# Kernel tuning notes

Hardware: AMD Instinct MI355X
Metric: run time of the kernel (lower is better)

## Reference

```python
import jax, jax.numpy as jnp
import numpy as np

SQRT_N = 64  # sqrt_n; padded sequence length n = SQRT_N**2 = 4096


def _perm(x, r):
    # rearrange '... (m n) -> ... (n m)' with m = n = r
    return x.reshape(*x.shape[:-1], r, r).swapaxes(-1, -2).reshape(x.shape)


def _blockdiag_matmul(x, w):
    # torch.einsum('bnm,...bm->...bn', w, x.view(..., b, m)).reshape(x.shape)
    b, _, m = w.shape
    xv = x.reshape(*x.shape[:-1], b, m)
    return jnp.einsum('bnm,...bm->...bn', w, xv).reshape(x.shape)


def _monarch(x, L, R, r):
    x = _perm(x, r)
    x = _blockdiag_matmul(x, L)
    x = _perm(x, r)
    x = _blockdiag_matmul(x, R)
    return _perm(x, r)


def setup_inputs() -> dict:
    key = jax.random.key(0)
    ks = jax.random.split(key, 9)
    B, S, H, D = 8, 4096, 8, 64
    r = SQRT_N
    bound_b = 1.0 / r
    # kaiming_uniform_(a=sqrt(5)) on a (r, r, r) tensor: fan_in = r*r,
    # gain = sqrt(2/(1+5)) = sqrt(1/3), bound = gain*sqrt(3/fan_in) = 1/r
    bound_w = 1.0 / r
    return {
        'queries': jax.random.normal(ks[0], (B, S, H, D), jnp.float32),
        'keys': jax.random.normal(ks[1], (B, S, H, D), jnp.float32),
        'values': jax.random.normal(ks[2], (B, S, H, D), jnp.float32),
        'M1L': jax.random.uniform(ks[3], (r, r, r), jnp.float32, -bound_w, bound_w),
        'M1R': jax.random.uniform(ks[4], (r, r, r), jnp.float32, -bound_w, bound_w),
        'M2L': jax.random.uniform(ks[5], (r, r, r), jnp.float32, -bound_w, bound_w),
        'M2R': jax.random.uniform(ks[6], (r, r, r), jnp.float32, -bound_w, bound_w),
        'b1': jax.random.uniform(ks[7], (r * r,), jnp.float32, -bound_b, bound_b),
        'b2': jax.random.uniform(ks[8], (r * r,), jnp.float32, -bound_b, bound_b),
    }


def reference(queries, keys, values, M1L, M1R, M2L, M2R, b1, b2):
    r = SQRT_N
    B, S, H, D = queries.shape
    n2 = r * r
    pad = n2 - S
    # (B,S,H,D) -> (B,H,D,S)
    q = jnp.transpose(queries, (0, 2, 3, 1))
    k = jnp.transpose(keys, (0, 2, 3, 1))
    v = jnp.transpose(values, (0, 2, 3, 1))
    cfg = [(0, 0)] * 3 + [(0, pad)]
    q = jnp.pad(q, cfg)
    k = jnp.pad(k, cfg)
    # A = M1(q) * k + b1 ; dropout is identity (eval / p=0)
    A = _monarch(q, M1L, M1R, r) * k + b1
    A = _monarch(A, M2L, M2R, r) + b2
    Y = A[..., :S] * v  # (B,H,D,S)
    return Y
```

## Files before the change

### kernel.cpp

```cpp
#include <hip/hip_runtime.h>
#include <cstdint>
#include <cstddef>

typedef unsigned short u16;
typedef __attribute__((ext_vector_type(8))) short bf16x8;
typedef __attribute__((ext_vector_type(4))) float f32x4;

#define S_LEN 4096

__device__ __forceinline__ float bf2f(u16 u) {
  return __uint_as_float(((unsigned)u) << 16);
}
__device__ __forceinline__ u16 f2bf(float f) {
  unsigned x = __float_as_uint(f);
  return (u16)((x + 0x7fffu + ((x >> 16) & 1u)) >> 16);
}

__device__ __forceinline__ int ltelem(int c, int r) {
  int swz = ((r >> 3) ^ (c & 7) ^ ((c >> 3) & 7)) & 7;
  return (c << 6) | (swz << 3) | (r & 7);
}

__device__ __forceinline__ bf16x8 load_afrag(const float* __restrict__ Wrow, int ks, int lane) {
  const float4* p = (const float4*)(Wrow + ks * 32 + ((lane >> 4) << 3));
  float4 a = p[0], b = p[1];
  bf16x8 r;
  r[0] = (short)f2bf(a.x); r[1] = (short)f2bf(a.y);
  r[2] = (short)f2bf(a.z); r[3] = (short)f2bf(a.w);
  r[4] = (short)f2bf(b.x); r[5] = (short)f2bf(b.y);
  r[6] = (short)f2bf(b.z); r[7] = (short)f2bf(b.w);
  return r;
}

__device__ __forceinline__ bf16x8 load_bfrag(const ushort* LT, int fc, int ks, int lane) {
  int c = (fc << 4) + (lane & 15);
  int kg = (ks << 2) + (lane >> 4);
  int base = (c << 6) | (((kg ^ (c & 7) ^ ((c >> 3) & 7)) & 7) << 3);
  return *(const bf16x8*)&LT[base];
}

__device__ __forceinline__ void mm16x64(const float* __restrict__ Arow, const ushort* LT,
                                        int lane, f32x4 acc[4]) {
#pragma unroll
  for (int ks = 0; ks < 2; ++ks) {
    bf16x8 af = load_afrag(Arow, ks, lane);
#pragma unroll
    for (int fc = 0; fc < 4; ++fc) {
      bf16x8 bf = load_bfrag(LT, fc, ks, lane);
      acc[fc] = __builtin_amdgcn_mfma_f32_16x16x32_bf16(af, bf, acc[fc], 0, 0, 0);
    }
  }
}

__global__ __launch_bounds__(256) void k_m1(const float* __restrict__ q,
                                            const float* __restrict__ L1,
                                            u16* __restrict__ T1) {
  const int B = blockIdx.x, bh = blockIdx.y;
  const int b = bh >> 3, h = bh & 7;
  __shared__ ushort LT[4096];
  const int tid = threadIdx.x, w = tid >> 6, lane = tid & 63;
  {
    const int m = tid >> 2, ch = tid & 3;
    const float* qrow = q + ((((size_t)b * S_LEN + (size_t)m * 64 + B) * 8 + h) << 6);
#pragma unroll
    for (int i = 0; i < 4; ++i) {
      float4 v = *(const float4*)(qrow + ch * 16 + i * 4);
      int c0 = ch * 16 + i * 4;
      LT[ltelem(c0 + 0, m)] = f2bf(v.x);
      LT[ltelem(c0 + 1, m)] = f2bf(v.y);
      LT[ltelem(c0 + 2, m)] = f2bf(v.z);
      LT[ltelem(c0 + 3, m)] = f2bf(v.w);
    }
  }
  __syncthreads();
  f32x4 acc[4] = {};
  mm16x64(L1 + (((size_t)B << 6) + (w << 4) + (lane & 15)) * 64, LT, lane, acc);
#pragma unroll
  for (int fc = 0; fc < 4; ++fc) {
    int d = (fc << 4) + (lane & 15);
#pragma unroll
    for (int r = 0; r < 4; ++r) {
      int n = (w << 4) + ((lane >> 4) << 2) + r;
      T1[(((size_t)bh * 64 + n) * 64 + B) * 64 + d] = f2bf(acc[fc][r]);
    }
  }
}

__global__ __launch_bounds__(256) void k_m2(const u16* __restrict__ T1,
                                            const float* __restrict__ R1,
                                            const float* __restrict__ L2,
                                            const float* __restrict__ keys,
                                            const float* __restrict__ b1,
                                            u16* __restrict__ T2) {
  const int o = blockIdx.x, bh = blockIdx.y;
  const int b = bh >> 3, h = bh & 7;
  __shared__ ushort LT[4096];
  __shared__ ushort LT2[4096];
  const int tid = threadIdx.x, w = tid >> 6, lane = tid & 63;
  const int rowi = tid >> 2, ch = tid & 3;
  for (int nl = 0; nl < 8; ++nl) {
    const int n = (o << 3) + nl;
    __syncthreads();
    {
      const u16* src = T1 + (((size_t)bh * 64 + n) * 64 + rowi) * 64 + ch * 16;
      u16 buf[16];
      *(uint4*)&buf[0] = *(const uint4*)(src);
      *(uint4*)&buf[8] = *(const uint4*)(src + 8);
#pragma unroll
      for (int e = 0; e < 16; ++e) LT[ltelem(ch * 16 + e, rowi)] = buf[e];
    }
    __syncthreads();
    f32x4 acc[4] = {};
    mm16x64(R1 + ((size_t)n * 64 + (w << 4) + (lane & 15)) * 64, LT, lane, acc);
    float b1v[4];
#pragma unroll
    for (int r = 0; r < 4; ++r)
      b1v[r] = b1[((w << 4) + ((lane >> 4) << 2) + r) * 64 + n];
#pragma unroll
    for (int fc = 0; fc < 4; ++fc) {
      int d = (fc << 4) + (lane & 15);
#pragma unroll
      for (int r = 0; r < 4; ++r) {
        int p = (w << 4) + ((lane >> 4) << 2) + r;
        float kv = keys[(((size_t)b * S_LEN + p * 64 + n) * 8 + h) * 64 + d];
        LT2[ltelem(d, p)] = f2bf(acc[fc][r] * kv + b1v[r]);
      }
    }
    __syncthreads();
    f32x4 acc2[4] = {};
    mm16x64(L2 + ((size_t)n * 64 + (w << 4) + (lane & 15)) * 64, LT2, lane, acc2);
#pragma unroll
    for (int fc = 0; fc < 4; ++fc) {
      int d = (fc << 4) + (lane & 15);
#pragma unroll
      for (int r = 0; r < 4; ++r) {
        int n2 = (w << 4) + ((lane >> 4) << 2) + r;
        T2[(((size_t)bh * 64 + n2) * 64 + n) * 64 + d] = f2bf(acc2[fc][r]);
      }
    }
  }
}

__global__ __launch_bounds__(256) void k_m3(const u16* __restrict__ T2,
                                            const float* __restrict__ R2,
                                            const float* __restrict__ vals,
                                            const float* __restrict__ b2,
                                            float* __restrict__ out) {
  const int o = blockIdx.x, bh = blockIdx.y;
  const int b = bh >> 3, h = bh & 7;
  __shared__ ushort LT[4096];
  __shared__ ushort SG[32768];
  const int tid = threadIdx.x, w = tid >> 6, lane = tid & 63;
  const int rowi = tid >> 2, ch = tid & 3;
  for (int nl = 0; nl < 8; ++nl) {
    const int np = (o << 3) + nl;
    __syncthreads();
    {
      const u16* src = T2 + (((size_t)bh * 64 + np) * 64 + rowi) * 64 + ch * 16;
      u16 buf[16];
      *(uint4*)&buf[0] = *(const uint4*)(src);
      *(uint4*)&buf[8] = *(const uint4*)(src + 8);
#pragma unroll
      for (int e = 0; e < 16; ++e) LT[ltelem(ch * 16 + e, rowi)] = buf[e];
    }
    __syncthreads();
    f32x4 acc[4] = {};
    mm16x64(R2 + ((size_t)np * 64 + (w << 4) + (lane & 15)) * 64, LT, lane, acc);
    float b2v[4];
#pragma unroll
    for (int r = 0; r < 4; ++r)
      b2v[r] = b2[((w << 4) + ((lane >> 4) << 2) + r) * 64 + np];
    int qw = nl >> 1;
#pragma unroll
    for (int fc = 0; fc < 4; ++fc) {
      int d = (fc << 4) + (lane & 15);
      int d43 = (d >> 3) & 3;
#pragma unroll
      for (int r = 0; r < 4; ++r) {
        int p = (w << 4) + ((lane >> 4) << 2) + r;
        float vv = vals[(((size_t)b * S_LEN + p * 64 + np) * 8 + h) * 64 + d];
        float y = (acc[fc][r] + b2v[r]) * vv;
        int g2 = (p >> 2) & 3;
        int pos = (qw ^ g2 ^ d43) & 3;
        SG[(((p << 6) + d) << 3) + pos * 2 + (nl & 1)] = f2bf(y);
      }
    }
  }
  __syncthreads();
#pragma unroll
  for (int it = 0; it < 16; ++it) {
    int cell = it * 256 + tid;
    int d = cell & 63, p = cell >> 6;
    int g2 = (p >> 2) & 3, d43 = (d >> 3) & 3;
    int base = ((p << 6) + d) << 3;
    float o8[8];
#pragma unroll
    for (int qd = 0; qd < 4; ++qd) {
      unsigned vv = *(const unsigned*)&SG[base + ((qd ^ g2 ^ d43) & 3) * 2];
      o8[qd * 2 + 0] = bf2f((u16)(vv & 0xffffu));
      o8[qd * 2 + 1] = bf2f((u16)(vv >> 16));
    }
    float* op = out + ((size_t)bh * 64 + d) * S_LEN + (p << 6) + (o << 3);
    float4 s0 = {o8[0], o8[1], o8[2], o8[3]};
    float4 s1 = {o8[4], o8[5], o8[6], o8[7]};
    *(float4*)op = s0;
    *(float4*)(op + 4) = s1;
  }
}

extern "C" void kernel_launch(void* const* d_in, const int* in_sizes, int n_in,
                              void* d_out, int out_size, void* d_ws, size_t ws_size,
                              hipStream_t stream) {
  const float* q   = (const float*)d_in[0];
  const float* k   = (const float*)d_in[1];
  const float* v   = (const float*)d_in[2];
  const float* M1L = (const float*)d_in[3];
  const float* M1R = (const float*)d_in[4];
  const float* M2L = (const float*)d_in[5];
  const float* M2R = (const float*)d_in[6];
  const float* b1  = (const float*)d_in[7];
  const float* b2  = (const float*)d_in[8];

  u16* T1 = (u16*)d_ws;
  u16* T2 = T1 + (size_t)64 * 64 * 64 * 64;

  dim3 blk(256);
  k_m1<<<dim3(64, 64), blk, 0, stream>>>(q, M1L, T1);
  k_m2<<<dim3(8, 64), blk, 0, stream>>>(T1, M1R, M2L, k, b1, T2);
  k_m3<<<dim3(8, 64), blk, 0, stream>>>(T2, M2R, v, b2, (float*)d_out);
}
```

Before: 135.5 us.

## Split monarch stages into one block per slice and add separate transpose kernel

k_m2 and k_m3 now assign one n-slice per block on a 64x64 grid instead of looping over 8 slices per block on an 8x64 grid, which raises parallelism. Keys and values are staged into shared memory with coalesced float4 loads and rounded to bf16 there, replacing per-element strided global reads. The final output transpose moves out of k_m3 into a new k_tr kernel that reads a bf16 intermediate reusing the T1 buffer. The trade-offs are an extra launch, an extra round trip of the intermediate through global memory, and rounding keys and values to bf16.

Result: faster. 116.1 us (-14.3%).

```diff
diff --git a/kernel.cpp b/kernel.cpp
--- a/kernel.cpp
+++ b/kernel.cpp
@@ -86,125 +86,139 @@
   }
 }
 
-__global__ __launch_bounds__(256) void k_m2(const u16* __restrict__ T1,
-                                            const float* __restrict__ R1,
-                                            const float* __restrict__ L2,
-                                            const float* __restrict__ keys,
-                                            const float* __restrict__ b1,
-                                            u16* __restrict__ T2) {
-  const int o = blockIdx.x, bh = blockIdx.y;
+__global__ __launch_bounds__(256) void k_m2b(const u16* __restrict__ T1,
+                                             const float* __restrict__ R1,
+                                             const float* __restrict__ L2,
+                                             const float* __restrict__ keys,
+                                             const float* __restrict__ b1,
+                                             u16* __restrict__ T2) {
+  const int n = blockIdx.x, bh = blockIdx.y;
   const int b = bh >> 3, h = bh & 7;
   __shared__ ushort LT[4096];
   __shared__ ushort LT2[4096];
+  __shared__ ushort KT[4096];
   const int tid = threadIdx.x, w = tid >> 6, lane = tid & 63;
-  const int rowi = tid >> 2, ch = tid & 3;
-  for (int nl = 0; nl < 8; ++nl) {
-    const int n = (o << 3) + nl;
-    __syncthreads();
-    {
-      const u16* src = T1 + (((size_t)bh * 64 + n) * 64 + rowi) * 64 + ch * 16;
-      u16 buf[16];
-      *(uint4*)&buf[0] = *(const uint4*)(src);
-      *(uint4*)&buf[8] = *(const uint4*)(src + 8);
-#pragma unroll
-      for (int e = 0; e < 16; ++e) LT[ltelem(ch * 16 + e, rowi)] = buf[e];
-    }
-    __syncthreads();
-    f32x4 acc[4] = {};
-    mm16x64(R1 + ((size_t)n * 64 + (w << 4) + (lane & 15)) * 64, LT, lane, acc);
-    float b1v[4];
-#pragma unroll
-    for (int r = 0; r < 4; ++r)
-      b1v[r] = b1[((w << 4) + ((lane >> 4) << 2) + r) * 64 + n];
-#pragma unroll
-    for (int fc = 0; fc < 4; ++fc) {
-      int d = (fc << 4) + (lane & 15);
-#pragma unroll
-      for (int r = 0; r < 4; ++r) {
-        int p = (w << 4) + ((lane >> 4) << 2) + r;
-        float kv = keys[(((size_t)b * S_LEN + p * 64 + n) * 8 + h) * 64 + d];
-        LT2[ltelem(d, p)] = f2bf(acc[fc][r] * kv + b1v[r]);
-      }
-    }
-    __syncthreads();
-    f32x4 acc2[4] = {};
-    mm16x64(L2 + ((size_t)n * 64 + (w << 4) + (lane & 15)) * 64, LT2, lane, acc2);
-#pragma unroll
-    for (int fc = 0; fc < 4; ++fc) {
-      int d = (fc << 4) + (lane & 15);
-#pragma unroll
-      for (int r = 0; r < 4; ++r) {
-        int n2 = (w << 4) + ((lane >> 4) << 2) + r;
-        T2[(((size_t)bh * 64 + n2) * 64 + n) * 64 + d] = f2bf(acc2[fc][r]);
-      }
-    }
-  }
-}
-
-__global__ __launch_bounds__(256) void k_m3(const u16* __restrict__ T2,
-                                            const float* __restrict__ R2,
-                                            const float* __restrict__ vals,
-                                            const float* __restrict__ b2,
-                                            float* __restrict__ out) {
-  const int o = blockIdx.x, bh = blockIdx.y;
+  {
+    const int rowi = tid >> 2, ch = tid & 3;
+    const u16* src = T1 + (((size_t)bh * 64 + n) * 64 + rowi) * 64 + ch * 16;
+    u16 buf[16];
+    *(uint4*)&buf[0] = *(const uint4*)(src);
+    *(uint4*)&buf[8] = *(const uint4*)(src + 8);
+#pragma unroll
+    for (int e = 0; e < 16; ++e) LT[ltelem(ch * 16 + e, rowi)] = buf[e];
+  }
+#pragma unroll
+  for (int i = 0; i < 4; ++i) {
+    int idx = i * 256 + tid;
+    int p = idx >> 4, c4 = (idx & 15) * 4;
+    float4 kv = *(const float4*)&keys[(((size_t)b * S_LEN + p * 64 + n) * 8 + h) * 64 + c4];
+    KT[ltelem(c4 + 0, p)] = f2bf(kv.x);
+    KT[ltelem(c4 + 1, p)] = f2bf(kv.y);
+    KT[ltelem(c4 + 2, p)] = f2bf(kv.z);
+    KT[ltelem(c4 + 3, p)] = f2bf(kv.w);
+  }
+  __syncthreads();
+  f32x4 acc[4] = {};
+  mm16x64(R1 + ((size_t)n * 64 + (w << 4) + (lane & 15)) * 64, LT, lane, acc);
+  float b1v[4];
+#pragma unroll
+  for (int r = 0; r < 4; ++r)
+    b1v[r] = b1[((w << 4) + ((lane >> 4) << 2) + r) * 64 + n];
+#pragma unroll
+  for (int fc = 0; fc < 4; ++fc) {
+    int d = (fc << 4) + (lane & 15);
+#pragma unroll
+    for (int r = 0; r < 4; ++r) {
+      int p = (w << 4) + ((lane >> 4) << 2) + r;
+      float kvv = bf2f(KT[ltelem(d, p)]);
+      LT2[ltelem(d, p)] = f2bf(acc[fc][r] * kvv + b1v[r]);
+    }
+  }
+  __syncthreads();
+  f32x4 acc2[4] = {};
+  mm16x64(L2 + ((size_t)n * 64 + (w << 4) + (lane & 15)) * 64, LT2, lane, acc2);
+#pragma unroll
+  for (int fc = 0; fc < 4; ++fc) {
+    int d = (fc << 4) + (lane & 15);
+#pragma unroll
+    for (int r = 0; r < 4; ++r) {
+      int n2 = (w << 4) + ((lane >> 4) << 2) + r;
+      T2[(((size_t)bh * 64 + n2) * 64 + n) * 64 + d] = f2bf(acc2[fc][r]);
+    }
+  }
+}
+
+__global__ __launch_bounds__(256) void k_m3b(const u16* __restrict__ T2,
+                                             const float* __restrict__ R2,
+                                             const float* __restrict__ vals,
+                                             const float* __restrict__ b2,
+                                             u16* __restrict__ Yp) {
+  const int np = blockIdx.x, bh = blockIdx.y;
   const int b = bh >> 3, h = bh & 7;
   __shared__ ushort LT[4096];
-  __shared__ ushort SG[32768];
+  __shared__ ushort VT[4096];
   const int tid = threadIdx.x, w = tid >> 6, lane = tid & 63;
-  const int rowi = tid >> 2, ch = tid & 3;
-  for (int nl = 0; nl < 8; ++nl) {
-    const int np = (o << 3) + nl;
-    __syncthreads();
-    {
-      const u16* src = T2 + (((size_t)bh * 64 + np) * 64 + rowi) * 64 + ch * 16;
-      u16 buf[16];
-      *(uint4*)&buf[0] = *(const uint4*)(src);
-      *(uint4*)&buf[8] = *(const uint4*)(src + 8);
-#pragma unroll
-      for (int e = 0; e < 16; ++e) LT[ltelem(ch * 16 + e, rowi)] = buf[e];
-    }
-    __syncthreads();
-    f32x4 acc[4] = {};
-    mm16x64(R2 + ((size_t)np * 64 + (w << 4) + (lane & 15)) * 64, LT, lane, acc);
-    float b2v[4];
-#pragma unroll
-    for (int r = 0; r < 4; ++r)
-      b2v[r] = b2[((w << 4) + ((lane >> 4) << 2) + r) * 64 + np];
-    int qw = nl >> 1;
-#pragma unroll
-    for (int fc = 0; fc < 4; ++fc) {
-      int d = (fc << 4) + (lane & 15);
-      int d43 = (d >> 3) & 3;
-#pragma unroll
-      for (int r = 0; r < 4; ++r) {
-        int p = (w << 4) + ((lane >> 4) << 2) + r;
-        float vv = vals[(((size_t)b * S_LEN + p * 64 + np) * 8 + h) * 64 + d];
-        float y = (acc[fc][r] + b2v[r]) * vv;
-        int g2 = (p >> 2) & 3;
-        int pos = (qw ^ g2 ^ d43) & 3;
-        SG[(((p << 6) + d) << 3) + pos * 2 + (nl & 1)] = f2bf(y);
-      }
-    }
-  }
-  __syncthreads();
-#pragma unroll
-  for (int it = 0; it < 16; ++it) {
-    int cell = it * 256 + tid;
-    int d = cell & 63, p = cell >> 6;
-    int g2 = (p >> 2) & 3, d43 = (d >> 3) & 3;
-    int base = ((p << 6) + d) << 3;
-    float o8[8];
-#pragma unroll
-    for (int qd = 0; qd < 4; ++qd) {
-      unsigned vv = *(const unsigned*)&SG[base + ((qd ^ g2 ^ d43) & 3) * 2];
-      o8[qd * 2 + 0] = bf2f((u16)(vv & 0xffffu));
-      o8[qd * 2 + 1] = bf2f((u16)(vv >> 16));
-    }
-    float* op = out + ((size_t)bh * 64 + d) * S_LEN + (p << 6) + (o << 3);
-    float4 s0 = {o8[0], o8[1], o8[2], o8[3]};
-    float4 s1 = {o8[4], o8[5], o8[6], o8[7]};
-    *(float4*)op = s0;
-    *(float4*)(op + 4) = s1;
+  {
+    const int rowi = tid >> 2, ch = tid & 3;
+    const u16* src = T2 + (((size_t)bh * 64 + np) * 64 + rowi) * 64 + ch * 16;
+    u16 buf[16];
+    *(uint4*)&buf[0] = *(const uint4*)(src);
+    *(uint4*)&buf[8] = *(const uint4*)(src + 8);
+#pragma unroll
+    for (int e = 0; e < 16; ++e) LT[ltelem(ch * 16 + e, rowi)] = buf[e];
+  }
+#pragma unroll
+  for (int i = 0; i < 4; ++i) {
+    int idx = i * 256 + tid;
+    int p = idx >> 4, c4 = (idx & 15) * 4;
+    float4 vv = *(const float4*)&vals[(((size_t)b * S_LEN + p * 64 + np) * 8 + h) * 64 + c4];
+    VT[ltelem(c4 + 0, p)] = f2bf(vv.x);
+    VT[ltelem(c4 + 1, p)] = f2bf(vv.y);
+    VT[ltelem(c4 + 2, p)] = f2bf(vv.z);
+    VT[ltelem(c4 + 3, p)] = f2bf(vv.w);
+  }
+  __syncthreads();
+  f32x4 acc[4] = {};
+  mm16x64(R2 + ((size_t)np * 64 + (w << 4) + (lane & 15)) * 64, LT, lane, acc);
+  float b2v[4];
+#pragma unroll
+  for (int r = 0; r < 4; ++r)
+    b2v[r] = b2[((w << 4) + ((lane >> 4) << 2) + r) * 64 + np];
+#pragma unroll
+  for (int fc = 0; fc < 4; ++fc) {
+    int d = (fc << 4) + (lane & 15);
+#pragma unroll
+    for (int r = 0; r < 4; ++r) {
+      int p = (w << 4) + ((lane >> 4) << 2) + r;
+      float vv = bf2f(VT[ltelem(d, p)]);
+      Yp[(((size_t)bh * 64 + np) * 64 + p) * 64 + d] = f2bf((acc[fc][r] + b2v[r]) * vv);
+    }
+  }
+}
+
+__global__ __launch_bounds__(256) void k_tr(const u16* __restrict__ Yp,
+                                            float* __restrict__ out) {
+  const int p = blockIdx.x, bh = blockIdx.y;
+  __shared__ ushort YT[4096];
+  const int tid = threadIdx.x;
+#pragma unroll
+  for (int i = 0; i < 2; ++i) {
+    int idx = i * 256 + tid;
+    int np = idx >> 3, q8 = idx & 7;
+    uint4 vv = *(const uint4*)&Yp[(((size_t)bh * 64 + np) * 64 + p) * 64 + q8 * 8];
+    *(uint4*)&YT[ltelem(np, q8 * 8)] = vv;
+  }
+  __syncthreads();
+#pragma unroll
+  for (int i = 0; i < 4; ++i) {
+    int idx = i * 256 + tid;
+    int d = idx >> 4, np0 = (idx & 15) * 4;
+    float4 o;
+    o.x = bf2f(YT[ltelem(np0 + 0, d)]);
+    o.y = bf2f(YT[ltelem(np0 + 1, d)]);
+    o.z = bf2f(YT[ltelem(np0 + 2, d)]);
+    o.w = bf2f(YT[ltelem(np0 + 3, d)]);
+    *(float4*)&out[((size_t)bh * 64 + d) * S_LEN + p * 64 + np0] = o;
   }
 }
 
@@ -223,9 +237,12 @@
 
   u16* T1 = (u16*)d_ws;
   u16* T2 = T1 + (size_t)64 * 64 * 64 * 64;
+  u16* Yp = T1;
 
   dim3 blk(256);
-  k_m1<<<dim3(64, 64), blk, 0, stream>>>(q, M1L, T1);
-  k_m2<<<dim3(8, 64), blk, 0, stream>>>(T1, M1R, M2L, k, b1, T2);
-  k_m3<<<dim3(8, 64), blk, 0, stream>>>(T2, M2R, v, b2, (float*)d_out);
-}
+  dim3 grd(64, 64);
+  k_m1 <<<grd, blk, 0, stream>>>(q, M1L, T1);
+  k_m2b<<<grd, blk, 0, stream>>>(T1, M1R, M2L, k, b1, T2);
+  k_m3b<<<grd, blk, 0, stream>>>(T2, M2R, v, b2, Yp);
+  k_tr <<<grd, blk, 0, stream>>>(Yp, (float*)d_out);
+}
```
